# Optimization experiments

Hardware: AMD Instinct MI355X
Metric: run time of the kernel (lower is better)

## Reference

```python
import jax, jax.numpy as jnp
import numpy as np

B = 4096   # batch
C = 1024   # per-node channels


def setup_inputs() -> dict:
    key = jax.random.key(0)
    k0, k1, k2, k3, k4 = jax.random.split(key, 5)
    x0 = jax.random.normal(k0, (B, C), dtype=jnp.float32)
    x1 = jax.random.normal(k1, (B, C), dtype=jnp.float32)
    # per-edge DNet weights: edge_in=concat (2 heads -> 2C) -> matmul W -> edge_out=split (2 tails of C)
    scale = 0.02
    W0 = jax.random.normal(k2, (2 * C, 2 * C), dtype=jnp.float32) * scale
    W1 = jax.random.normal(k3, (2 * C, 2 * C), dtype=jnp.float32) * scale
    W2 = jax.random.normal(k4, (2 * C, 2 * C), dtype=jnp.float32) * scale
    return {"x0": x0, "x1": x1, "W0": W0, "W1": W1, "W2": W2}


def _edge(head_a, head_b, W):
    # MHD_concat over sorted head nodes (dim=1), DNet matmul, MHD_split into tail node channels
    z = jnp.concatenate([head_a, head_b], axis=1) @ W  # [B, 2C]
    return z[:, :C], z[:, C:]  # two tail tensors [B, C]


def reference(x0, x1, W0, W1, W2):
    # DAG routing in topological order (MHD_topological_sort of the role matrix):
    # edge0: heads (n0, n1) -> tails (n2, n3)
    # edge1: heads (n2, n3) -> tails (n4, n5)
    # edge2: heads (n4, n5) -> tails (n6, n7)
    # node_tail_func = 'sum' (single contribution per tail here)
    n2, n3 = _edge(x0, x1, W0)
    n4, n5 = _edge(n2, n3, W1)
    n6, n7 = _edge(n4, n5, W2)
    # output: concat of terminal nodes (sorted order)
    return jnp.concatenate([n6, n7], axis=1)  # [B, 2C]
```

## Files before the change

kernel.cpp:

```cpp
#include <hip/hip_runtime.h>
#include <hip/hip_bf16.h>
#include <stdint.h>

typedef __bf16 bf16;
typedef __bf16 bf16x8 __attribute__((ext_vector_type(8)));
typedef float f32x4 __attribute__((ext_vector_type(4)));

#define GAS __attribute__((address_space(1)))
#define LAS __attribute__((address_space(3)))

static constexpr int M = 4096;
static constexpr int N = 2048;
static constexpr int K = 2048;

static constexpr int BM = 128, BN = 256, BK = 64;
static constexpr int NT = K / BK;
static constexpr int A_ELE = BM * BK;
static constexpr int B_ELE = BN * BK;
static constexpr int BUF_ELE = A_ELE + B_ELE;

static constexpr int WA_ELE = 64 * BK;
static constexpr int WB_ELE = 128 * BK;
static constexpr int WBUF_ELE = WA_ELE + WB_ELE;
static constexpr int WGRID = 512;

__device__ __forceinline__ void gload_lds16(const bf16* gsrc, bf16* ldst) {
    __builtin_amdgcn_global_load_lds((const GAS void*)gsrc, (LAS void*)ldst, 16, 0, 0);
}

__device__ __forceinline__ void pack8(const float* __restrict__ src, bf16* __restrict__ dst) {
    float4 v0 = *reinterpret_cast<const float4*>(src);
    float4 v1 = *reinterpret_cast<const float4*>(src + 4);
    bf16x8 o;
    o[0] = (bf16)v0.x; o[1] = (bf16)v0.y; o[2] = (bf16)v0.z; o[3] = (bf16)v0.w;
    o[4] = (bf16)v1.x; o[5] = (bf16)v1.y; o[6] = (bf16)v1.z; o[7] = (bf16)v1.w;
    *reinterpret_cast<bf16x8*>(dst) = o;
}

__device__ __forceinline__ void transpose_tile(const float* __restrict__ W, bf16* __restrict__ Wt,
                                               int t, int tid, bf16 (*tile)[33]) {
    int n0 = (t & 63) * 32;
    int k0 = (t >> 6) * 32;
    int tx = tid & 31;
    int ty = tid >> 5;
    #pragma unroll
    for (int i = 0; i < 4; i++) {
        int k = ty + i * 8;
        tile[k][tx] = (bf16)W[(size_t)(k0 + k) * N + n0 + tx];
    }
    __syncthreads();
    #pragma unroll
    for (int i = 0; i < 4; i++) {
        int n = ty + i * 8;
        Wt[(size_t)(n0 + n) * K + k0 + tx] = tile[tx][n];
    }
}

__device__ __forceinline__ void gemmw_body(const bf16* __restrict__ A,
                                           const bf16* __restrict__ Bt,
                                           bf16* __restrict__ C,
                                           int bid, bf16* lds) {
    int swz = (bid & 7) * (WGRID >> 3) + (bid >> 3);
    int tm = swz >> 4;
    int tn = swz & 15;

    int tid  = threadIdx.x;
    int wave = tid >> 6;
    int lane = tid & 63;
    int wr = wave >> 1;
    int wc = wave & 1;
    int fr = lane & 15;
    int fb = lane >> 4;

    int srow = tid >> 3;
    int scol = ((tid & 7) ^ (srow & 7)) * 8;
    const bf16* aS = A  + (size_t)(tm * 64  + srow) * K + scol;
    const bf16* bS = Bt + (size_t)(tn * 128 + srow) * K + scol;
    int sdst = wave * 512;

    int aoff  = (wr * 32 + fr) * 64;
    int boff  = (wc * 64 + fr) * 64;
    int slot0 = ((fb) ^ (fr & 7)) * 8;
    int slot1 = ((4 | fb) ^ (fr & 7)) * 8;

    f32x4 acc[2][4] = {};
    bf16x8 af0[2], bv0[4], af1[2], bv1[4];

    auto STAGE = [&](int bi, int t) {
        bf16* ba = lds + bi * WBUF_ELE;
        bf16* bb = ba + WA_ELE;
        const bf16* a = aS + t * BK;
        const bf16* b = bS + t * BK;
        gload_lds16(a,          ba + sdst);
        gload_lds16(a + 32 * K, ba + sdst + 2048);
        #pragma unroll
        for (int c = 0; c < 4; c++)
            gload_lds16(b + (size_t)c * 32 * K, bb + sdst + c * 2048);
    };
    auto READ = [&](const bf16* ba, const bf16* bb, int slot, bf16x8 af[2], bf16x8 bv[4]) {
        af[0] = *reinterpret_cast<const bf16x8*>(ba + aoff + slot);
        af[1] = *reinterpret_cast<const bf16x8*>(ba + aoff + 1024 + slot);
        #pragma unroll
        for (int ni = 0; ni < 4; ni++)
            bv[ni] = *reinterpret_cast<const bf16x8*>(bb + boff + ni * 1024 + slot);
    };
    auto MFMA8 = [&](const bf16x8 af[2], const bf16x8 bv[4]) {
        #pragma unroll
        for (int mi = 0; mi < 2; mi++)
            #pragma unroll
            for (int ni = 0; ni < 4; ni++)
                acc[mi][ni] = __builtin_amdgcn_mfma_f32_16x16x32_bf16(af[mi], bv[ni], acc[mi][ni], 0, 0, 0);
    };
    auto TILE = [&](int t, int cb, int sb) {
        const bf16* ba = lds + cb * WBUF_ELE;
        const bf16* bb = ba + WA_ELE;
        READ(ba, bb, slot0, af0, bv0);
        READ(ba, bb, slot1, af1, bv1);
        STAGE(sb, t + 2);
        __builtin_amdgcn_s_setprio(1);
        MFMA8(af0, bv0);
        MFMA8(af1, bv1);
        __builtin_amdgcn_s_setprio(0);
        asm volatile("s_waitcnt lgkmcnt(0)" ::: "memory");
        asm volatile("s_waitcnt vmcnt(6)" ::: "memory");
        __builtin_amdgcn_s_barrier();
    };

    STAGE(0, 0);
    STAGE(1, 1);
    asm volatile("s_waitcnt vmcnt(6)" ::: "memory");
    __builtin_amdgcn_s_barrier();

    for (int i = 0; i < 10; ++i) {
        TILE(3 * i,     0, 2);
        TILE(3 * i + 1, 1, 0);
        TILE(3 * i + 2, 2, 1);
    }
    {
        const bf16* ba = lds;
        const bf16* bb = ba + WA_ELE;
        READ(ba, bb, slot0, af0, bv0);
        READ(ba, bb, slot1, af1, bv1);
        MFMA8(af0, bv0);
        MFMA8(af1, bv1);
        asm volatile("s_waitcnt lgkmcnt(0)" ::: "memory");
        asm volatile("s_waitcnt vmcnt(0)" ::: "memory");
        __builtin_amdgcn_s_barrier();
    }
    {
        const bf16* ba = lds + WBUF_ELE;
        const bf16* bb = ba + WA_ELE;
        READ(ba, bb, slot0, af0, bv0);
        READ(ba, bb, slot1, af1, bv1);
        MFMA8(af0, bv0);
        MFMA8(af1, bv1);
    }

    int row0 = tm * 64 + wr * 32 + (lane >> 4) * 4;
    int col0 = tn * 128 + wc * 64 + fr;
    #pragma unroll
    for (int mi = 0; mi < 2; mi++)
        #pragma unroll
        for (int r = 0; r < 4; r++) {
            size_t base = (size_t)(row0 + mi * 16 + r) * 2048 + col0;
            #pragma unroll
            for (int ni = 0; ni < 4; ni++)
                C[base + ni * 16] = (bf16)acc[mi][ni][r];
        }
}

__global__ __launch_bounds__(256) void k1_prep(const float* __restrict__ W0, bf16* __restrict__ W0pk,
                                               const float* __restrict__ W1, bf16* __restrict__ W1t) {
    __shared__ bf16 tile[32][33];
    int bid = blockIdx.x;
    int tid = threadIdx.x;
    if (bid < 2048) {
        int idx = (bid * 256 + tid) * 8;
        pack8(W0 + idx, W0pk + idx);
    } else {
        transpose_tile(W1, W1t, bid - 2048, tid, tile);
    }
}

__global__ __launch_bounds__(256, 2) void g1_fused(const bf16* __restrict__ A, const bf16* __restrict__ Bt,
                                                   bf16* __restrict__ C,
                                                   const float* __restrict__ W2, bf16* __restrict__ W2t) {
    __shared__ bf16 lds[3 * WBUF_ELE];
    int bid = blockIdx.x;
    if (bid < WGRID) {
        gemmw_body(A, Bt, C, bid, lds);
    } else {
        transpose_tile(W2, W2t, bid - WGRID, threadIdx.x, (bf16(*)[33])lds);
    }
}

__global__ __launch_bounds__(256, 2) void g2_fused(const bf16* __restrict__ A, const bf16* __restrict__ Bt,
                                                   bf16* __restrict__ C,
                                                   const float* __restrict__ x0, const float* __restrict__ x1,
                                                   bf16* __restrict__ Xpk) {
    __shared__ bf16 lds[3 * WBUF_ELE];
    int bid = blockIdx.x;
    if (bid < WGRID) {
        gemmw_body(A, Bt, C, bid, lds);
    } else {
        int idx = ((bid - WGRID) * 256 + threadIdx.x) * 8;
        int b = idx >> 11;
        int c = idx & 2047;
        const float* src = (c < 1024) ? (x0 + (size_t)b * 1024 + c)
                                      : (x1 + (size_t)b * 1024 + (c - 1024));
        pack8(src, Xpk + idx);
    }
}

__global__ __launch_bounds__(512, 2) void gemmx_kernel(const bf16* __restrict__ A,
                                                       const bf16* __restrict__ Bt,
                                                       float* __restrict__ Cout) {
    __shared__ bf16 lds[3 * BUF_ELE];

    int bid = blockIdx.x;
    int cpx = gridDim.x >> 3;
    int swz = (bid & 7) * cpx + (bid >> 3);
    int tm = swz >> 3;
    int tn = swz & 7;

    int tid  = threadIdx.x;
    int wave = tid >> 6;
    int lane = tid & 63;
    int wr = wave >> 2;
    int wc = wave & 3;
    int fr = lane & 15;
    int fb = lane >> 4;

    int srow = wave * 8 + (lane >> 3);
    int scol = ((lane & 7) ^ (lane >> 3)) * 8;
    const bf16* aS = A  + (size_t)(tm * BM + srow) * K + scol;
    const bf16* bS = Bt + (size_t)(tn * BN + srow) * K + scol;
    int sdst = wave * 512;

    int aoff  = (wr * 64 + fr) * 64;
    int boff  = (wc * 64 + fr) * 64;
    int slot0 = ((fb) ^ (fr & 7)) * 8;
    int slot1 = ((4 | fb) ^ (fr & 7)) * 8;

    f32x4 acc[4][4] = {};
    bf16x8 af0[4], bv0[4], af1[4], bv1[4];

    auto STAGE = [&](int bi, int t) {
        bf16* ba = (bf16*)lds + bi * BUF_ELE;
        bf16* bb = ba + A_ELE;
        const bf16* a = aS + t * BK;
        const bf16* b = bS + t * BK;
        gload_lds16(a,           ba + sdst);
        gload_lds16(a + 64 * K,  ba + sdst + 4096);
        gload_lds16(b,           bb + sdst);
        gload_lds16(b + 64 * K,  bb + sdst + 4096);
        gload_lds16(b + 128 * K, bb + sdst + 8192);
        gload_lds16(b + 192 * K, bb + sdst + 12288);
    };
    auto READ = [&](const bf16* ba, const bf16* bb, int slot, bf16x8 af[4], bf16x8 bv[4]) {
        #pragma unroll
        for (int mi = 0; mi < 4; mi++)
            af[mi] = *reinterpret_cast<const bf16x8*>(ba + aoff + mi * 1024 + slot);
        #pragma unroll
        for (int ni = 0; ni < 4; ni++)
            bv[ni] = *reinterpret_cast<const bf16x8*>(bb + boff + ni * 1024 + slot);
    };
    auto MFMA16 = [&](const bf16x8 af[4], const bf16x8 bv[4]) {
        #pragma unroll
        for (int mi = 0; mi < 4; mi++)
            #pragma unroll
            for (int ni = 0; ni < 4; ni++)
                acc[mi][ni] = __builtin_amdgcn_mfma_f32_16x16x32_bf16(af[mi], bv[ni], acc[mi][ni], 0, 0, 0);
    };
    auto TILE = [&](int t, int cb, int sb) {
        const bf16* ba = (const bf16*)lds + cb * BUF_ELE;
        const bf16* bb = ba + A_ELE;
        READ(ba, bb, slot0, af0, bv0);
        READ(ba, bb, slot1, af1, bv1);
        STAGE(sb, t + 2);
        __builtin_amdgcn_s_setprio(1);
        MFMA16(af0, bv0);
        MFMA16(af1, bv1);
        __builtin_amdgcn_s_setprio(0);
        asm volatile("s_waitcnt lgkmcnt(0)" ::: "memory");
        asm volatile("s_waitcnt vmcnt(6)" ::: "memory");
        __builtin_amdgcn_s_barrier();
    };

    STAGE(0, 0);
    STAGE(1, 1);
    asm volatile("s_waitcnt vmcnt(6)" ::: "memory");
    __builtin_amdgcn_s_barrier();

    for (int i = 0; i < 10; ++i) {
        TILE(3 * i,     0, 2);
        TILE(3 * i + 1, 1, 0);
        TILE(3 * i + 2, 2, 1);
    }
    {
        const bf16* ba = (const bf16*)lds;
        const bf16* bb = ba + A_ELE;
        READ(ba, bb, slot0, af0, bv0);
        READ(ba, bb, slot1, af1, bv1);
        MFMA16(af0, bv0);
        MFMA16(af1, bv1);
        asm volatile("s_waitcnt lgkmcnt(0)" ::: "memory");
        asm volatile("s_waitcnt vmcnt(0)" ::: "memory");
        __builtin_amdgcn_s_barrier();
    }
    {
        const bf16* ba = (const bf16*)lds + BUF_ELE;
        const bf16* bb = ba + A_ELE;
        READ(ba, bb, slot0, af0, bv0);
        READ(ba, bb, slot1, af1, bv1);
        MFMA16(af0, bv0);
        MFMA16(af1, bv1);
    }

    int row0 = tm * BM + wr * 64 + (lane >> 4) * 4;
    int col0 = tn * BN + wc * 64 + (lane & 15);
    #pragma unroll
    for (int mi = 0; mi < 4; mi++)
        #pragma unroll
        for (int r = 0; r < 4; r++) {
            size_t base = (size_t)(row0 + mi * 16 + r) * N + col0;
            #pragma unroll
            for (int ni = 0; ni < 4; ni++)
                Cout[base + ni * 16] = acc[mi][ni][r];
        }
}

extern "C" void kernel_launch(void* const* d_in, const int* in_sizes, int n_in,
                              void* d_out, int out_size, void* d_ws, size_t ws_size,
                              hipStream_t stream) {
    const float* x0 = (const float*)d_in[0];
    const float* x1 = (const float*)d_in[1];
    const float* W0 = (const float*)d_in[2];
    const float* W1 = (const float*)d_in[3];
    const float* W2 = (const float*)d_in[4];

    char* ws = (char*)d_ws;
    const size_t MB = 1024 * 1024;
    bf16* Xpk    = (bf16*)(ws + 0 * MB);
    bf16* W1t    = (bf16*)(ws + 16 * MB);
    bf16* W012t  = (bf16*)(ws + 16 * MB);
    bf16* W2t    = (bf16*)(ws + 24 * MB);
    bf16* W01    = (bf16*)(ws + 32 * MB);
    bf16* W0pk   = (bf16*)d_out;

    k1_prep<<<2048 + 4096, 256, 0, stream>>>(W0, W0pk, W1, W1t);
    g1_fused<<<WGRID + 4096, 256, 0, stream>>>(W0pk, W1t, W01, W2, W2t);
    g2_fused<<<WGRID + 4096, 256, 0, stream>>>(W2t, W01, W012t, x0, x1, Xpk);
    gemmx_kernel<<<(M / BM) * (N / BN), 512, 0, stream>>>(Xpk, W012t, (float*)d_out);
}
```

Measured before the change: 101.2 us.

## Split K across wave halves with 64x128 wave tiles and LDS reduction

Reorganizes the 8 waves so each half of the block processes one half of the BK=64 slice, with every wave computing a 64x128 output tile (4x8 MFMAs) instead of 64x64 over the full BK. This raises the MFMA-to-LDS-read ratio per wave, since each A fragment is reused across 8 B fragments. Partial sums from the upper half are reduced through LDS at the end before the store. In exchange it doubles the accumulator registers, which risks occupancy under launch_bounds(512,2), and adds an epilogue reduction step in LDS.

```diff
diff --git a/kernel.cpp b/kernel.cpp
--- a/kernel.cpp
+++ b/kernel.cpp
@@ -226,8 +226,9 @@
     int tid  = threadIdx.x;
     int wave = tid >> 6;
     int lane = tid & 63;
-    int wr = wave >> 2;
-    int wc = wave & 3;
+    int kh = wave >> 2;
+    int wr = (wave >> 1) & 1;
+    int wc = wave & 1;
     int fr = lane & 15;
     int fb = lane >> 4;
 
@@ -237,13 +238,12 @@
     const bf16* bS = Bt + (size_t)(tn * BN + srow) * K + scol;
     int sdst = wave * 512;
 
-    int aoff  = (wr * 64 + fr) * 64;
-    int boff  = (wc * 64 + fr) * 64;
-    int slot0 = ((fb) ^ (fr & 7)) * 8;
-    int slot1 = ((4 | fb) ^ (fr & 7)) * 8;
-
-    f32x4 acc[4][4] = {};
-    bf16x8 af0[4], bv0[4], af1[4], bv1[4];
+    int aoff = (wr * 64 + fr) * 64;
+    int boff = (wc * 128 + fr) * 64;
+    int slot = (((kh << 2) | fb) ^ (fr & 7)) * 8;
+
+    f32x4 acc[4][8] = {};
+    bf16x8 af[4], bv[8];
 
     auto STAGE = [&](int bi, int t) {
         bf16* ba = (bf16*)lds + bi * BUF_ELE;
@@ -257,30 +257,28 @@
         gload_lds16(b + 128 * K, bb + sdst + 8192);
         gload_lds16(b + 192 * K, bb + sdst + 12288);
     };
-    auto READ = [&](const bf16* ba, const bf16* bb, int slot, bf16x8 af[4], bf16x8 bv[4]) {
+    auto READ = [&](const bf16* ba, const bf16* bb) {
         #pragma unroll
         for (int mi = 0; mi < 4; mi++)
             af[mi] = *reinterpret_cast<const bf16x8*>(ba + aoff + mi * 1024 + slot);
         #pragma unroll
-        for (int ni = 0; ni < 4; ni++)
+        for (int ni = 0; ni < 8; ni++)
             bv[ni] = *reinterpret_cast<const bf16x8*>(bb + boff + ni * 1024 + slot);
     };
-    auto MFMA16 = [&](const bf16x8 af[4], const bf16x8 bv[4]) {
+    auto MFMA32 = [&]() {
         #pragma unroll
         for (int mi = 0; mi < 4; mi++)
             #pragma unroll
-            for (int ni = 0; ni < 4; ni++)
+            for (int ni = 0; ni < 8; ni++)
                 acc[mi][ni] = __builtin_amdgcn_mfma_f32_16x16x32_bf16(af[mi], bv[ni], acc[mi][ni], 0, 0, 0);
     };
     auto TILE = [&](int t, int cb, int sb) {
         const bf16* ba = (const bf16*)lds + cb * BUF_ELE;
         const bf16* bb = ba + A_ELE;
-        READ(ba, bb, slot0, af0, bv0);
-        READ(ba, bb, slot1, af1, bv1);
+        READ(ba, bb);
         STAGE(sb, t + 2);
         __builtin_amdgcn_s_setprio(1);
-        MFMA16(af0, bv0);
-        MFMA16(af1, bv1);
+        MFMA32();
         __builtin_amdgcn_s_setprio(0);
         asm volatile("s_waitcnt lgkmcnt(0)" ::: "memory");
         asm volatile("s_waitcnt vmcnt(6)" ::: "memory");
@@ -300,10 +298,8 @@
     {
         const bf16* ba = (const bf16*)lds;
         const bf16* bb = ba + A_ELE;
-        READ(ba, bb, slot0, af0, bv0);
-        READ(ba, bb, slot1, af1, bv1);
-        MFMA16(af0, bv0);
-        MFMA16(af1, bv1);
+        READ(ba, bb);
+        MFMA32();
         asm volatile("s_waitcnt lgkmcnt(0)" ::: "memory");
         asm volatile("s_waitcnt vmcnt(0)" ::: "memory");
         __builtin_amdgcn_s_barrier();
@@ -311,23 +307,43 @@
     {
         const bf16* ba = (const bf16*)lds + BUF_ELE;
         const bf16* bb = ba + A_ELE;
-        READ(ba, bb, slot0, af0, bv0);
-        READ(ba, bb, slot1, af1, bv1);
-        MFMA16(af0, bv0);
-        MFMA16(af1, bv1);
-    }
-
-    int row0 = tm * BM + wr * 64 + (lane >> 4) * 4;
-    int col0 = tn * BN + wc * 64 + (lane & 15);
-    #pragma unroll
-    for (int mi = 0; mi < 4; mi++)
-        #pragma unroll
-        for (int r = 0; r < 4; r++) {
-            size_t base = (size_t)(row0 + mi * 16 + r) * N + col0;
-            #pragma unroll
-            for (int ni = 0; ni < 4; ni++)
-                Cout[base + ni * 16] = acc[mi][ni][r];
+        READ(ba, bb);
+        MFMA32();
+    }
+
+    asm volatile("s_waitcnt lgkmcnt(0)" ::: "memory");
+    __builtin_amdgcn_s_barrier();
+
+    float* red = (float*)lds;
+    int pair = wave & 3;
+    if (kh) {
+        #pragma unroll
+        for (int mi = 0; mi < 4; mi++)
+            #pragma unroll
+            for (int ni = 0; ni < 8; ni++)
+                *reinterpret_cast<f32x4*>(red + (size_t)4 * (pair * 2048 + (mi * 8 + ni) * 64 + lane)) = acc[mi][ni];
+    }
+    asm volatile("s_waitcnt lgkmcnt(0)" ::: "memory");
+    __builtin_amdgcn_s_barrier();
+    if (!kh) {
+        int row0 = tm * BM + wr * 64 + (lane >> 4) * 4;
+        int col0 = tn * BN + wc * 128 + fr;
+        #pragma unroll
+        for (int mi = 0; mi < 4; mi++) {
+            #pragma unroll
+            for (int ni = 0; ni < 8; ni++) {
+                f32x4 o = *reinterpret_cast<const f32x4*>(red + (size_t)4 * (pair * 2048 + (mi * 8 + ni) * 64 + lane));
+                acc[mi][ni] += o;
+            }
+            #pragma unroll
+            for (int r = 0; r < 4; r++) {
+                size_t base = (size_t)(row0 + mi * 16 + r) * N + col0;
+                #pragma unroll
+                for (int ni = 0; ni < 8; ni++)
+                    Cout[base + ni * 16] = acc[mi][ni][r];
+            }
         }
+    }
 }
 
 extern "C" void kernel_launch(void* const* d_in, const int* in_sizes, int n_in,
```

Result: no change. 102.0 us (+0.8%).

## Software-pipeline LDS fragment reads one tile ahead in final GEMM

Applied to the files above, without the earlier changes.

Restructures the final-edge GEMM main loop so that register fragments for the next K-tile are read from LDS while the MFMAs for the current tile's already-loaded fragments run. Two fragment sets alternate between tiles, and the prologue now stages three tiles. sched_barriers pin the instruction order. This aims to hide LDS read latency behind MFMA issue, but it doubles fragment register usage, which may cause spills or lower occupancy and raises the risk of an off-by-one error in the buffer rotation.

```diff
diff --git a/kernel.cpp b/kernel.cpp
--- a/kernel.cpp
+++ b/kernel.cpp
@@ -212,10 +212,15 @@
     }
 }
 
+struct Frags { bf16x8 a0[4], a1[4], b0[4], b1[4]; };
+
 __global__ __launch_bounds__(512, 2) void gemmx_kernel(const bf16* __restrict__ A,
                                                        const bf16* __restrict__ Bt,
                                                        float* __restrict__ Cout) {
     __shared__ bf16 lds[3 * BUF_ELE];
+    bf16* B0 = (bf16*)lds;
+    bf16* B1 = B0 + BUF_ELE;
+    bf16* B2 = B1 + BUF_ELE;
 
     int bid = blockIdx.x;
     int cpx = gridDim.x >> 3;
@@ -243,11 +248,11 @@
     int slot1 = ((4 | fb) ^ (fr & 7)) * 8;
 
     f32x4 acc[4][4] = {};
-    bf16x8 af0[4], bv0[4], af1[4], bv1[4];
-
-    auto STAGE = [&](int bi, int t) {
-        bf16* ba = (bf16*)lds + bi * BUF_ELE;
-        bf16* bb = ba + A_ELE;
+    Frags fA, fB;
+
+    auto STAGE = [&](bf16* buf, int t) {
+        bf16* ba = buf;
+        bf16* bb = buf + A_ELE;
         const bf16* a = aS + t * BK;
         const bf16* b = bS + t * BK;
         gload_lds16(a,           ba + sdst);
@@ -257,65 +262,91 @@
         gload_lds16(b + 128 * K, bb + sdst + 8192);
         gload_lds16(b + 192 * K, bb + sdst + 12288);
     };
-    auto READ = [&](const bf16* ba, const bf16* bb, int slot, bf16x8 af[4], bf16x8 bv[4]) {
+    auto READS = [&](const bf16* buf, Frags& f) {
+        const bf16* ba = buf;
+        const bf16* bb = buf + A_ELE;
+        #pragma unroll
+        for (int mi = 0; mi < 4; mi++) {
+            f.a0[mi] = *reinterpret_cast<const bf16x8*>(ba + aoff + mi * 1024 + slot0);
+            f.a1[mi] = *reinterpret_cast<const bf16x8*>(ba + aoff + mi * 1024 + slot1);
+        }
+        #pragma unroll
+        for (int ni = 0; ni < 4; ni++) {
+            f.b0[ni] = *reinterpret_cast<const bf16x8*>(bb + boff + ni * 1024 + slot0);
+            f.b1[ni] = *reinterpret_cast<const bf16x8*>(bb + boff + ni * 1024 + slot1);
+        }
+    };
+    auto MFMA32 = [&](const Frags& f) {
+        __builtin_amdgcn_s_setprio(1);
         #pragma unroll
         for (int mi = 0; mi < 4; mi++)
-            af[mi] = *reinterpret_cast<const bf16x8*>(ba + aoff + mi * 1024 + slot);
-        #pragma unroll
-        for (int ni = 0; ni < 4; ni++)
-            bv[ni] = *reinterpret_cast<const bf16x8*>(bb + boff + ni * 1024 + slot);
-    };
-    auto MFMA16 = [&](const bf16x8 af[4], const bf16x8 bv[4]) {
+            #pragma unroll
+            for (int ni = 0; ni < 4; ni++)
+                acc[mi][ni] = __builtin_amdgcn_mfma_f32_16x16x32_bf16(f.a0[mi], f.b0[ni], acc[mi][ni], 0, 0, 0);
         #pragma unroll
         for (int mi = 0; mi < 4; mi++)
             #pragma unroll
             for (int ni = 0; ni < 4; ni++)
-                acc[mi][ni] = __builtin_amdgcn_mfma_f32_16x16x32_bf16(af[mi], bv[ni], acc[mi][ni], 0, 0, 0);
-    };
-    auto TILE = [&](int t, int cb, int sb) {
-        const bf16* ba = (const bf16*)lds + cb * BUF_ELE;
-        const bf16* bb = ba + A_ELE;
-        READ(ba, bb, slot0, af0, bv0);
-        READ(ba, bb, slot1, af1, bv1);
-        STAGE(sb, t + 2);
-        __builtin_amdgcn_s_setprio(1);
-        MFMA16(af0, bv0);
-        MFMA16(af1, bv1);
+                acc[mi][ni] = __builtin_amdgcn_mfma_f32_16x16x32_bf16(f.a1[mi], f.b1[ni], acc[mi][ni], 0, 0, 0);
         __builtin_amdgcn_s_setprio(0);
+    };
+    auto SYNC6 = [&]() {
         asm volatile("s_waitcnt lgkmcnt(0)" ::: "memory");
         asm volatile("s_waitcnt vmcnt(6)" ::: "memory");
         __builtin_amdgcn_s_barrier();
     };
-
-    STAGE(0, 0);
-    STAGE(1, 1);
+    auto TILE_A = [&](bf16* bufR, bf16* bufS, int ts) {
+        READS(bufR, fB);
+        __builtin_amdgcn_sched_barrier(0);
+        STAGE(bufS, ts);
+        __builtin_amdgcn_sched_barrier(0);
+        MFMA32(fA);
+        SYNC6();
+    };
+    auto TILE_B = [&](bf16* bufR, bf16* bufS, int ts) {
+        READS(bufR, fA);
+        __builtin_amdgcn_sched_barrier(0);
+        STAGE(bufS, ts);
+        __builtin_amdgcn_sched_barrier(0);
+        MFMA32(fB);
+        SYNC6();
+    };
+
+    STAGE(B0, 0);
+    STAGE(B1, 1);
+    STAGE(B2, 2);
     asm volatile("s_waitcnt vmcnt(6)" ::: "memory");
     __builtin_amdgcn_s_barrier();
-
-    for (int i = 0; i < 10; ++i) {
-        TILE(3 * i,     0, 2);
-        TILE(3 * i + 1, 1, 0);
-        TILE(3 * i + 2, 2, 1);
-    }
+    READS(B0, fA);
+
+    for (int i = 0; i < 4; ++i) {
+        int t = 6 * i;
+        TILE_A(B1, B0, t + 3);
+        TILE_B(B2, B1, t + 4);
+        TILE_A(B0, B2, t + 5);
+        TILE_B(B1, B0, t + 6);
+        TILE_A(B2, B1, t + 7);
+        TILE_B(B0, B2, t + 8);
+    }
+    TILE_A(B1, B0, 27);
+    TILE_B(B2, B1, 28);
+    TILE_A(B0, B2, 29);
+    TILE_B(B1, B0, 30);
+    TILE_A(B2, B1, 31);
     {
-        const bf16* ba = (const bf16*)lds;
-        const bf16* bb = ba + A_ELE;
-        READ(ba, bb, slot0, af0, bv0);
-        READ(ba, bb, slot1, af1, bv1);
-        MFMA16(af0, bv0);
-        MFMA16(af1, bv1);
+        READS(B0, fA);
+        __builtin_amdgcn_sched_barrier(0);
+        MFMA32(fB);
         asm volatile("s_waitcnt lgkmcnt(0)" ::: "memory");
         asm volatile("s_waitcnt vmcnt(0)" ::: "memory");
         __builtin_amdgcn_s_barrier();
     }
     {
-        const bf16* ba = (const bf16*)lds + BUF_ELE;
-        const bf16* bb = ba + A_ELE;
-        READ(ba, bb, slot0, af0, bv0);
-        READ(ba, bb, slot1, af1, bv1);
-        MFMA16(af0, bv0);
-        MFMA16(af1, bv1);
-    }
+        READS(B1, fB);
+        __builtin_amdgcn_sched_barrier(0);
+        MFMA32(fA);
+    }
+    MFMA32(fB);
 
     int row0 = tm * BM + wr * 64 + (lane >> 4) * 4;
     int col0 = tn * BN + wc * 64 + (lane & 15);
```

Result: no change. 100.1 us, median of 2 (-1.0%).

## Split GEMM k-tile into four barrier-fenced phases interleaving LDS reads, loads, MFMAs

Applied to the files above, without the earlier changes.

Restructures the main-loop k-tile of the bf16 GEMM so that, instead of reading all fragments, issuing all six global->LDS loads and then running 32 MFMAs, each tile runs as four sub-phases. Each sub-phase reads a few fragments, issues part of the prefetch loads and runs 8 MFMAs at raised priority, with workgroup barriers and sched_barriers between phases. The intent is to interleave LDS reads, global prefetch and matrix work across waves in a ping-pong style and to lower register pressure from holding both fragment sets. The cost is many more barriers per tile, which can stall waves if the phases are not balanced.

```diff
diff --git a/kernel.cpp b/kernel.cpp
--- a/kernel.cpp
+++ b/kernel.cpp
@@ -243,79 +243,103 @@
     int slot1 = ((4 | fb) ^ (fr & 7)) * 8;
 
     f32x4 acc[4][4] = {};
-    bf16x8 af0[4], bv0[4], af1[4], bv1[4];
-
-    auto STAGE = [&](int bi, int t) {
-        bf16* ba = (bf16*)lds + bi * BUF_ELE;
-        bf16* bb = ba + A_ELE;
+
+    #define BAR()     __builtin_amdgcn_s_barrier()
+    #define LGKM0()   do { asm volatile("s_waitcnt lgkmcnt(0)" ::: "memory"); \
+                           __builtin_amdgcn_sched_barrier(0); } while (0)
+
+    auto MFMA2x4 = [&](int m0, const bf16x8 af[2], const bf16x8 bv[4]) {
+        __builtin_amdgcn_s_setprio(1);
+        #pragma unroll
+        for (int mi = 0; mi < 2; mi++)
+            #pragma unroll
+            for (int ni = 0; ni < 4; ni++)
+                acc[m0 + mi][ni] = __builtin_amdgcn_mfma_f32_16x16x32_bf16(af[mi], bv[ni], acc[m0 + mi][ni], 0, 0, 0);
+        __builtin_amdgcn_s_setprio(0);
+    };
+
+    auto KTILE = [&](const bf16* buf, bf16* sbuf, int st, int vm, bool dostage) {
+        const bf16* ba = buf;
+        const bf16* bb = buf + A_ELE;
+        const bf16* ag = aS + st * BK;
+        const bf16* bg = bS + st * BK;
+        bf16x8 aP[2], aQ[2], bV[4];
+
+        aP[0] = *reinterpret_cast<const bf16x8*>(ba + aoff + slot0);
+        aP[1] = *reinterpret_cast<const bf16x8*>(ba + aoff + 1024 + slot0);
+        #pragma unroll
+        for (int ni = 0; ni < 4; ni++)
+            bV[ni] = *reinterpret_cast<const bf16x8*>(bb + boff + ni * 1024 + slot0);
+        if (dostage) {
+            gload_lds16(ag,          sbuf + sdst);
+            gload_lds16(ag + 64 * K, sbuf + sdst + 4096);
+        }
+        BAR(); LGKM0();
+        MFMA2x4(0, aP, bV);
+        BAR();
+
+        aQ[0] = *reinterpret_cast<const bf16x8*>(ba + aoff + 2048 + slot0);
+        aQ[1] = *reinterpret_cast<const bf16x8*>(ba + aoff + 3072 + slot0);
+        if (dostage) {
+            gload_lds16(bg,          sbuf + A_ELE + sdst);
+            gload_lds16(bg + 64 * K, sbuf + A_ELE + sdst + 4096);
+        }
+        BAR(); LGKM0();
+        MFMA2x4(2, aQ, bV);
+        BAR();
+
+        aP[0] = *reinterpret_cast<const bf16x8*>(ba + aoff + slot1);
+        aP[1] = *reinterpret_cast<const bf16x8*>(ba + aoff + 1024 + slot1);
+        #pragma unroll
+        for (int ni = 0; ni < 4; ni++)
+            bV[ni] = *reinterpret_cast<const bf16x8*>(bb + boff + ni * 1024 + slot1);
+        if (dostage) {
+            gload_lds16(bg + 128 * K, sbuf + A_ELE + sdst + 8192);
+            gload_lds16(bg + 192 * K, sbuf + A_ELE + sdst + 12288);
+        }
+        BAR(); LGKM0();
+        MFMA2x4(0, aP, bV);
+        BAR();
+
+        aQ[0] = *reinterpret_cast<const bf16x8*>(ba + aoff + 2048 + slot1);
+        aQ[1] = *reinterpret_cast<const bf16x8*>(ba + aoff + 3072 + slot1);
+        BAR(); LGKM0();
+        MFMA2x4(2, aQ, bV);
+        if (vm == 6)      asm volatile("s_waitcnt vmcnt(6)" ::: "memory");
+        else if (vm == 0) asm volatile("s_waitcnt vmcnt(0)" ::: "memory");
+        if (vm >= 0) BAR();
+    };
+
+    bf16* B0 = (bf16*)lds;
+    bf16* B1 = B0 + BUF_ELE;
+    bf16* B2 = B1 + BUF_ELE;
+
+    auto STAGE_ALL = [&](bf16* buf, int t) {
         const bf16* a = aS + t * BK;
         const bf16* b = bS + t * BK;
-        gload_lds16(a,           ba + sdst);
-        gload_lds16(a + 64 * K,  ba + sdst + 4096);
-        gload_lds16(b,           bb + sdst);
-        gload_lds16(b + 64 * K,  bb + sdst + 4096);
-        gload_lds16(b + 128 * K, bb + sdst + 8192);
-        gload_lds16(b + 192 * K, bb + sdst + 12288);
-    };
-    auto READ = [&](const bf16* ba, const bf16* bb, int slot, bf16x8 af[4], bf16x8 bv[4]) {
-        #pragma unroll
-        for (int mi = 0; mi < 4; mi++)
-            af[mi] = *reinterpret_cast<const bf16x8*>(ba + aoff + mi * 1024 + slot);
-        #pragma unroll
-        for (int ni = 0; ni < 4; ni++)
-            bv[ni] = *reinterpret_cast<const bf16x8*>(bb + boff + ni * 1024 + slot);
-    };
-    auto MFMA16 = [&](const bf16x8 af[4], const bf16x8 bv[4]) {
-        #pragma unroll
-        for (int mi = 0; mi < 4; mi++)
-            #pragma unroll
-            for (int ni = 0; ni < 4; ni++)
-                acc[mi][ni] = __builtin_amdgcn_mfma_f32_16x16x32_bf16(af[mi], bv[ni], acc[mi][ni], 0, 0, 0);
-    };
-    auto TILE = [&](int t, int cb, int sb) {
-        const bf16* ba = (const bf16*)lds + cb * BUF_ELE;
-        const bf16* bb = ba + A_ELE;
-        READ(ba, bb, slot0, af0, bv0);
-        READ(ba, bb, slot1, af1, bv1);
-        STAGE(sb, t + 2);
-        __builtin_amdgcn_s_setprio(1);
-        MFMA16(af0, bv0);
-        MFMA16(af1, bv1);
-        __builtin_amdgcn_s_setprio(0);
-        asm volatile("s_waitcnt lgkmcnt(0)" ::: "memory");
-        asm volatile("s_waitcnt vmcnt(6)" ::: "memory");
-        __builtin_amdgcn_s_barrier();
-    };
-
-    STAGE(0, 0);
-    STAGE(1, 1);
+        gload_lds16(a,           buf + sdst);
+        gload_lds16(a + 64 * K,  buf + sdst + 4096);
+        gload_lds16(b,           buf + A_ELE + sdst);
+        gload_lds16(b + 64 * K,  buf + A_ELE + sdst + 4096);
+        gload_lds16(b + 128 * K, buf + A_ELE + sdst + 8192);
+        gload_lds16(b + 192 * K, buf + A_ELE + sdst + 12288);
+    };
+
+    STAGE_ALL(B0, 0);
+    STAGE_ALL(B1, 1);
     asm volatile("s_waitcnt vmcnt(6)" ::: "memory");
     __builtin_amdgcn_s_barrier();
 
     for (int i = 0; i < 10; ++i) {
-        TILE(3 * i,     0, 2);
-        TILE(3 * i + 1, 1, 0);
-        TILE(3 * i + 2, 2, 1);
-    }
-    {
-        const bf16* ba = (const bf16*)lds;
-        const bf16* bb = ba + A_ELE;
-        READ(ba, bb, slot0, af0, bv0);
-        READ(ba, bb, slot1, af1, bv1);
-        MFMA16(af0, bv0);
-        MFMA16(af1, bv1);
-        asm volatile("s_waitcnt lgkmcnt(0)" ::: "memory");
-        asm volatile("s_waitcnt vmcnt(0)" ::: "memory");
-        __builtin_amdgcn_s_barrier();
-    }
-    {
-        const bf16* ba = (const bf16*)lds + BUF_ELE;
-        const bf16* bb = ba + A_ELE;
-        READ(ba, bb, slot0, af0, bv0);
-        READ(ba, bb, slot1, af1, bv1);
-        MFMA16(af0, bv0);
-        MFMA16(af1, bv1);
-    }
+        KTILE(B0, B2, 3 * i + 2, 6, true);
+        KTILE(B1, B0, 3 * i + 3, 6, true);
+        KTILE(B2, B1, 3 * i + 4, 6, true);
+    }
+    KTILE(B0, nullptr, 0, 0, false);
+    KTILE(B1, nullptr, 0, -1, false);
+
+    #undef BAR
+    #undef LGKM0
 
     int row0 = tm * BM + wr * 64 + (lane >> 4) * 4;
     int col0 = tn * BN + wc * 64 + (lane & 15);
```

Result: no change. 102.7 us (+1.5%).
